# Kernel optimization log

Measured on AMD Instinct MI355X. Metric: run time of the kernel, lower is better.

Reference implementation:

```python
import jax, jax.numpy as jnp
import numpy as np

DIM, HEADS, DEPTH, SEQ, LOCAL_W = 1024, 16, 7, 2048, 64
HEAD_DIM = DIM // HEADS
SCALE = 1.0 / HEAD_DIM ** 0.5


def cantor_mask(S, depth, local_window):
    """Allowed (i,j): |i-j| within local window, OR |i-j| lies in the Cantor set
    under `depth` levels of ternary subdivision (no base-3 digit equals 1)."""
    idx = np.arange(S)
    d = np.abs(idx[:, None] - idx[None, :])
    x = d.copy()
    ok = np.ones_like(d, dtype=bool)
    for _ in range(depth):
        ok &= (x % 3) != 1
        x //= 3
    ok &= x == 0  # offset must be < 3**depth
    return jnp.asarray(ok | (d <= local_window))  # [S, S] bool


def setup_inputs() -> dict:
    key = jax.random.key(0)
    ks = jax.random.split(key, 8)
    B = 2
    s = 0.02
    return {
        "query": jax.random.normal(ks[0], (B, SEQ, DIM), jnp.float32),
        "key_value": jax.random.normal(ks[1], (B, SEQ, DIM), jnp.float32),
        "Wq": jax.random.normal(ks[2], (DIM, DIM), jnp.float32) * s,
        "bq": jnp.zeros((DIM,), jnp.float32),
        "Wkv": jax.random.normal(ks[3], (DIM, 2 * DIM), jnp.float32) * s,
        "bkv": jnp.zeros((2 * DIM,), jnp.float32),
        "Wo": jax.random.normal(ks[4], (DIM, DIM), jnp.float32) * s,
        "bo": jnp.zeros((DIM,), jnp.float32),
    }


def reference(query, key_value, Wq, bq, Wkv, bkv, Wo, bo):
    B, S, D = query.shape
    H, hd = HEADS, HEAD_DIM
    mask = cantor_mask(S, DEPTH, LOCAL_W)  # static [S, S] bool

    q = (query @ Wq + bq).reshape(B, S, H, hd).transpose(0, 2, 1, 3)  # [B,H,S,hd]
    kv = (key_value @ Wkv + bkv).reshape(B, S, 2, H, hd).transpose(2, 0, 3, 1, 4)
    k, v = kv[0], kv[1]  # [B,H,S,hd]

    scores = jnp.einsum("bhqd,bhkd->bhqk", q, k) * SCALE
    scores = jnp.where(mask, scores, jnp.finfo(scores.dtype).min)
    attn = jax.nn.softmax(scores, axis=-1)
    out = jnp.einsum("bhqk,bhkd->bhqd", attn, v)  # [B,H,S,hd]
    out = out.transpose(0, 2, 1, 3).reshape(B, S, D)
    return out @ Wo + bo
```

## Files before the change

kernel.cpp:

```cpp
#include <hip/hip_runtime.h>
#include <stdint.h>

typedef _Float16 half_t;
typedef __attribute__((ext_vector_type(8))) _Float16 half8;
typedef __attribute__((ext_vector_type(4))) _Float16 half4;
typedef __attribute__((ext_vector_type(4))) float floatx4;

#define SEQ 2048
#define NH 16
#define HD 64

#define MFMA16(a, b, c) __builtin_amdgcn_mfma_f32_16x16x16f16(a, b, c, 0, 0, 0)
#define MFMA32K(a, b, c) __builtin_amdgcn_mfma_f32_16x16x32_f16(a, b, c, 0, 0, 0)

#define QSCALE 0.1803368801111306f

__global__ __launch_bounds__(256) void prep(
    const float* __restrict__ query, const float* __restrict__ key_value,
    const float* __restrict__ Wq, const float* __restrict__ Wkv,
    const float* __restrict__ Wo, half_t* __restrict__ xq,
    half_t* __restrict__ xkv, half_t* __restrict__ wqT,
    half_t* __restrict__ wkvT, half_t* __restrict__ woT,
    uint8_t* __restrict__ tok, uint8_t* __restrict__ tok16,
    uint64_t* __restrict__ maskw) {
  int bx = blockIdx.x, tid = threadIdx.x;
  if (bx < 2048) {
    const float* s; half_t* d; int base;
    if (bx < 1024) { s = query; d = xq; base = bx * 4096; }
    else { s = key_value; d = xkv; base = (bx - 1024) * 4096; }
#pragma unroll
    for (int u = 0; u < 4; ++u) {
      int i = base + u * 1024 + tid * 4;
      floatx4 v = *(const floatx4*)(s + i);
      half4 h;
      h[0] = (half_t)v[0]; h[1] = (half_t)v[1];
      h[2] = (half_t)v[2]; h[3] = (half_t)v[3];
      *(half4*)(d + i) = h;
    }
    return;
  }
  if (bx < 4096) {
    __shared__ float tile[32][33];
    int tx = tid & 31, ty = tid >> 5;
    const int K = 1024;
#pragma unroll
    for (int u = 0; u < 2; ++u) {
      int t = (bx - 2048) * 2 + u;
      const float* W; half_t* Wt; int N, nt, kt;
      if (t < 1024) { W = Wq; Wt = wqT; N = 1024; nt = t & 31; kt = t >> 5; }
      else if (t < 3072) { int t2 = t - 1024; W = Wkv; Wt = wkvT; N = 2048; nt = t2 & 63; kt = t2 >> 6; }
      else { int t2 = t - 3072; W = Wo; Wt = woT; N = 1024; nt = t2 & 31; kt = t2 >> 5; }
      int n0 = nt * 32, k0 = kt * 32;
#pragma unroll
      for (int i = 0; i < 4; ++i)
        tile[ty + i * 8][tx] = W[(size_t)(k0 + ty + i * 8) * N + n0 + tx];
      __syncthreads();
#pragma unroll
      for (int i = 0; i < 4; ++i)
        Wt[(size_t)(n0 + ty + i * 8) * K + k0 + tx] = (half_t)tile[tx][ty + i * 8];
      __syncthreads();
    }
    return;
  }
  __shared__ uint8_t slut[2048];
  int ib = bx - 4096;
  for (int d = tid; d < 2048; d += 256) {
    int x = d;
    bool ok = true;
    for (int it = 0; it < 7; ++it) { ok &= ((x % 3) != 1); x /= 3; }
    ok &= (x == 0);
    slut[d] = (ok || d <= 64) ? 1 : 0;
  }
  __syncthreads();
  if (ib == 0) {
    if (tid < 64) {
      int delta = tid - 32;
      int lo = delta * 64 - 63, hi = delta * 64 + 63;
      uint8_t any = 0;
      for (int x = lo; x <= hi; ++x) {
        int a = x < 0 ? -x : x;
        if (a < 2048) any |= slut[a];
      }
      tok[tid] = any;
    }
    {
      int d16 = tid - 128;
      int ctr = d16 * 16;
      uint8_t any = 0;
      for (int x = ctr - 15; x <= ctr + 15; ++x) {
        int a = x < 0 ? -x : x;
        if (a < 2048) any |= slut[a];
      }
      tok16[tid] = any;
    }
  }
  int g = ib * 256 + tid;
  int tt = g - 2048;
  uint64_t w = 0;
  for (int jj = 0; jj < 64; ++jj) {
    int d = tt - jj; d = d < 0 ? -d : d;
    if (d < 2048 && slut[d]) w |= (1ull << jj);
  }
  maskw[g] = w;
}

__device__ __forceinline__ void cp16(half_t* lds, const half_t* g) {
  __builtin_amdgcn_global_load_lds(
      (const __attribute__((address_space(1))) uint32_t*)g,
      (__attribute__((address_space(3))) uint32_t*)lds, 16, 0, 0);
}

__global__ __launch_bounds__(256) void gemm_qkv(
    const half_t* __restrict__ xq, const half_t* __restrict__ xkv,
    const half_t* __restrict__ wqT, const half_t* __restrict__ wkvT,
    const float* __restrict__ bq, const float* __restrict__ bkv,
    half_t* __restrict__ qout, half_t* __restrict__ kout,
    half_t* __restrict__ vTout) {
  extern __shared__ char smemraw[];
  half_t* As = (half_t*)smemraw;
  half_t* Bs = As + 8192;
  const int K = 1024;
  bool isq = blockIdx.y < 8;
  const half_t* A = isq ? xq : xkv;
  const half_t* Bt = isq ? wqT : wkvT;
  const float* bias = isq ? bq : bkv;
  int n0 = (isq ? blockIdx.y : (blockIdx.y - 8)) * 128;
  int m0 = blockIdx.x * 128;

  int tid = threadIdx.x;
  int wave = tid >> 6, lane = tid & 63;
  int c = lane & 15, quad = lane >> 4;
  int wm = (wave >> 1) * 64, wn = (wave & 1) * 64;

  floatx4 acc[4][4] = {};
  int arow = tid >> 2, akc = (tid & 3) * 8;

  cp16(&As[wave * 512], A + (size_t)(m0 + arow) * K + akc);
  cp16(&As[2048 + wave * 512], A + (size_t)(m0 + 64 + arow) * K + akc);
  cp16(&Bs[wave * 512], Bt + (size_t)(n0 + arow) * K + akc);
  cp16(&Bs[2048 + wave * 512], Bt + (size_t)(n0 + 64 + arow) * K + akc);

  for (int kt = 0; kt < 32; ++kt) {
    __syncthreads();
    if (kt + 1 < 32) {
      int k0 = (kt + 1) * 32;
      int b = (kt + 1) & 1;
      cp16(&As[b * 4096 + wave * 512], A + (size_t)(m0 + arow) * K + k0 + akc);
      cp16(&As[b * 4096 + 2048 + wave * 512], A + (size_t)(m0 + 64 + arow) * K + k0 + akc);
      cp16(&Bs[b * 4096 + wave * 512], Bt + (size_t)(n0 + arow) * K + k0 + akc);
      cp16(&Bs[b * 4096 + 2048 + wave * 512], Bt + (size_t)(n0 + 64 + arow) * K + k0 + akc);
    }
    int b = kt & 1;
    half8 af[4], bf[4];
#pragma unroll
    for (int mt = 0; mt < 4; ++mt)
      af[mt] = *(const half8*)&As[b * 4096 + (wm + mt * 16 + c) * 32 + quad * 8];
#pragma unroll
    for (int nt = 0; nt < 4; ++nt)
      bf[nt] = *(const half8*)&Bs[b * 4096 + (wn + nt * 16 + c) * 32 + quad * 8];
#pragma unroll
    for (int mt = 0; mt < 4; ++mt)
#pragma unroll
      for (int nt = 0; nt < 4; ++nt)
        acc[mt][nt] = MFMA32K(af[mt], bf[nt], acc[mt][nt]);
  }

  __syncthreads();
  half_t* ep = (half_t*)smemraw;
  int bb = m0 >> 11, sbase = m0 & 2047;
  bool isv = (!isq) && (n0 >= 1024);

  if (!isv) {
#pragma unroll
    for (int nt = 0; nt < 4; ++nt) {
      int nl = wn + nt * 16 + c;
      float bv = bias[n0 + nl];
#pragma unroll
      for (int mt = 0; mt < 4; ++mt)
#pragma unroll
        for (int r = 0; r < 4; ++r) {
          int ml = wm + mt * 16 + quad * 4 + r;
          float v = acc[mt][nt][r] + bv;
          if (isq) v *= QSCALE;
          ep[ml * 128 + nl] = (half_t)v;
        }
    }
    __syncthreads();
    half_t* outp = isq ? qout : kout;
#pragma unroll
    for (int rd = 0; rd < 8; ++rd) {
      int id = rd * 256 + tid;
      int ml = id >> 4, ch = id & 15;
      int ng = n0 + ch * 8;
      int h = ng >> 6, d0 = ng & 63;
      half8 v = *(const half8*)&ep[ml * 128 + ch * 8];
      *(half8*)(outp + ((size_t)(bb * 16 + h) * SEQ + sbase + ml) * 64 + d0) = v;
    }
  } else {
#pragma unroll
    for (int nt = 0; nt < 4; ++nt) {
      int nl = wn + nt * 16 + c;
      float bv = bias[n0 + nl];
#pragma unroll
      for (int mt = 0; mt < 4; ++mt) {
        int ml = wm + mt * 16 + quad * 4;
        half4 hv;
#pragma unroll
        for (int r = 0; r < 4; ++r) hv[r] = (half_t)(acc[mt][nt][r] + bv);
        *(half4*)&ep[nl * 136 + ml] = hv;
      }
    }
    __syncthreads();
#pragma unroll
    for (int rd = 0; rd < 8; ++rd) {
      int id = rd * 256 + tid;
      int nl = id >> 4, mc = id & 15;
      int ng = n0 + nl;
      int h = (ng >> 6) & 15, d = ng & 63;
      half8 v = *(const half8*)&ep[nl * 136 + mc * 8];
      *(half8*)(vTout + ((size_t)(bb * 16 + h) * 64 + d) * SEQ + sbase + mc * 8) = v;
    }
  }
}

__global__ __launch_bounds__(256) void gemm_out(
    const half_t* __restrict__ A, const half_t* __restrict__ Bt,
    const float* __restrict__ bias, float* __restrict__ outf) {
  __shared__ half_t As[2][128 * 32];
  __shared__ half_t Bs[2][64 * 32];
  const int K = 1024;
  int tid = threadIdx.x;
  int wave = tid >> 6, lane = tid & 63;
  int c = lane & 15, quad = lane >> 4;
  int wm = (wave >> 1) * 64, wn = (wave & 1) * 32;
  int m0 = blockIdx.x * 128, n0 = blockIdx.y * 64;

  floatx4 acc[4][2] = {};
  int arow = tid >> 2, akc = (tid & 3) * 8;

  cp16(&As[0][wave * 512], A + (size_t)(m0 + arow) * K + akc);
  cp16(&As[0][2048 + wave * 512], A + (size_t)(m0 + 64 + arow) * K + akc);
  cp16(&Bs[0][wave * 512], Bt + (size_t)(n0 + arow) * K + akc);

  for (int kt = 0; kt < 32; ++kt) {
    __syncthreads();
    if (kt + 1 < 32) {
      int k0 = (kt + 1) * 32;
      int b = (kt + 1) & 1;
      cp16(&As[b][wave * 512], A + (size_t)(m0 + arow) * K + k0 + akc);
      cp16(&As[b][2048 + wave * 512], A + (size_t)(m0 + 64 + arow) * K + k0 + akc);
      cp16(&Bs[b][wave * 512], Bt + (size_t)(n0 + arow) * K + k0 + akc);
    }
    int b = kt & 1;
    half8 af[4], bf[2];
#pragma unroll
    for (int mt = 0; mt < 4; ++mt)
      af[mt] = *(const half8*)&As[b][(wm + mt * 16 + c) * 32 + quad * 8];
#pragma unroll
    for (int nt = 0; nt < 2; ++nt)
      bf[nt] = *(const half8*)&Bs[b][(wn + nt * 16 + c) * 32 + quad * 8];
#pragma unroll
    for (int mt = 0; mt < 4; ++mt)
#pragma unroll
      for (int nt = 0; nt < 2; ++nt)
        acc[mt][nt] = MFMA32K(af[mt], bf[nt], acc[mt][nt]);
  }

#pragma unroll
  for (int nt = 0; nt < 2; ++nt) {
    int n = n0 + wn + nt * 16 + c;
    float bv = bias[n];
#pragma unroll
    for (int mt = 0; mt < 4; ++mt)
#pragma unroll
      for (int r = 0; r < 4; ++r) {
        int m = m0 + wm + mt * 16 + quad * 4 + r;
        outf[(size_t)m * 1024 + n] = acc[mt][nt][r] + bv;
      }
  }
}

__global__ __launch_bounds__(512) void attn_kernel(
    const half_t* __restrict__ qb, const half_t* __restrict__ kb,
    const half_t* __restrict__ vTg, half_t* __restrict__ ctx,
    const uint64_t* __restrict__ maskw, const uint8_t* __restrict__ tok,
    const uint8_t* __restrict__ tok16g) {
  __shared__ half_t kT[64 * 64];
  __shared__ half_t vT[64 * 64];
  __shared__ half_t ot[128 * 72];
  __shared__ int list[34];
  __shared__ uint8_t tok16s[256];

  int tid = threadIdx.x, wave = tid >> 6, lane = tid & 63;
  int c = lane & 15, q = lane >> 4;
  int id = blockIdx.x;
  int bh = (id & 7) * 4 + ((id >> 3) & 3);
  int it128 = id >> 5;
  int i0 = it128 << 7;
  const half_t* qbase = qb + (size_t)bh * SEQ * HD;
  const half_t* kg = kb + (size_t)bh * SEQ * HD;
  const half_t* vg = vTg + (size_t)bh * HD * SEQ;

  if (tid < 256) tok16s[tid] = tok16g[tid];
  if (wave == 0) {
    int jt = lane;
    int base = i0 >> 6;
    bool act = (jt < 32) &&
               (tok[(jt - base) + 32] | tok[(jt - base - 1) + 32]);
    unsigned long long bal = __ballot(act);
    if (act) {
      int pre = __popcll(bal & ((1ull << jt) - 1));
      list[1 + pre] = jt << 6;
    }
    if (lane == 0) list[0] = __popcll(bal);
  }

  int i_row = i0 + wave * 16 + c;
  int it16 = (i0 >> 4) + wave;
  half8 qf0 = *(const half8*)(qbase + (size_t)i_row * 64 + q * 8);
  half8 qf1 = *(const half8*)(qbase + (size_t)i_row * 64 + 32 + q * 8);

  floatx4 oacc[4] = {};
  floatx4 lacc = {};
  half4 ones;
  ones[0] = (half_t)1.f; ones[1] = (half_t)1.f;
  ones[2] = (half_t)1.f; ones[3] = (half_t)1.f;

  int srow = tid >> 3;
  int sch = tid & 7;
  int ssw = srow & 7;

  __syncthreads();
  int nact = list[0];
  int j0 = list[1];

  half8 kr = *(const half8*)(kg + (size_t)(j0 + srow) * 64 + sch * 8);
  half8 vr = *(const half8*)(vg + (size_t)srow * SEQ + j0 + sch * 8);

  for (int ti = 0; ti < nact; ++ti) {
    uint64_t w = maskw[(i_row - j0) + 2048];
    int bidx = (j0 >> 4) - it16 + 128;
    __syncthreads();
    *(half8*)&kT[srow * 64 + ((sch ^ ssw) * 8)] = kr;
    *(half8*)&vT[srow * 64 + ((sch ^ ssw) * 8)] = vr;
    int j0n = j0;
    if (ti + 1 < nact) {
      j0n = list[2 + ti];
      kr = *(const half8*)(kg + (size_t)(j0n + srow) * 64 + sch * 8);
      vr = *(const half8*)(vg + (size_t)srow * SEQ + j0n + sch * 8);
    }
    __syncthreads();

    uint32_t wlo = (uint32_t)(w >> (4 * q));
    uint32_t whi = (uint32_t)(w >> (32 + 4 * q));
#pragma unroll
    for (int jt = 0; jt < 4; ++jt) {
      if (!tok16s[bidx + jt]) continue;
      int row = jt * 16 + c;
      int sw = c & 7;
      half8 a0 = *(const half8*)&kT[row * 64 + ((q ^ sw) * 8)];
      half8 a1 = *(const half8*)&kT[row * 64 + (((4 + q) ^ sw) * 8)];
      floatx4 t = {};
      t = MFMA32K(a0, qf0, t);
      t = MFMA32K(a1, qf1, t);
      uint32_t ww = (jt < 2) ? wlo : whi;
#pragma unroll
      for (int r = 0; r < 4; ++r) {
        float p = __builtin_exp2f(t[r]);
        int bitpos = 16 * (jt & 1) + r;
        uint32_t msk = (uint32_t)(((int)(ww << (31 - bitpos))) >> 31);
        t[r] = __uint_as_float(__float_as_uint(p) & msk);
      }
      auto lo = __builtin_amdgcn_cvt_pkrtz(t[0], t[1]);
      auto hi = __builtin_amdgcn_cvt_pkrtz(t[2], t[3]);
      half4 pb;
      pb[0] = lo[0]; pb[1] = lo[1]; pb[2] = hi[0]; pb[3] = hi[1];
      lacc = MFMA16(ones, pb, lacc);
#pragma unroll
      for (int mt = 0; mt < 4; ++mt) {
        int drow = mt * 16 + c;
        int ch = 2 * jt + (q >> 1);
        half4 a = *(const half4*)&vT[drow * 64 + ((ch ^ sw) * 8) + (q & 1) * 4];
        oacc[mt] = MFMA16(a, pb, oacc[mt]);
      }
    }
    j0 = j0n;
  }

  float inv_l = 1.0f / lacc[0];
#pragma unroll
  for (int mt = 0; mt < 4; ++mt)
#pragma unroll
    for (int r = 0; r < 4; ++r)
      ot[(wave * 16 + c) * 72 + mt * 16 + 4 * q + r] = (half_t)(oacc[mt][r] * inv_l);
  __syncthreads();
  {
    int row = tid >> 2, chq = tid & 3;
    int b = bh >> 4, h = bh & 15;
    size_t base = (((size_t)(b * SEQ + i0 + row) * NH) + h) * 64 + chq * 16;
    half8 v0 = *(const half8*)&ot[row * 72 + chq * 16];
    half8 v1 = *(const half8*)&ot[row * 72 + chq * 16 + 8];
    *(half8*)(ctx + base) = v0;
    *(half8*)(ctx + base + 8) = v1;
  }
}

extern "C" void kernel_launch(void* const* d_in, const int* in_sizes, int n_in,
                              void* d_out, int out_size, void* d_ws, size_t ws_size,
                              hipStream_t stream) {
  const float* query = (const float*)d_in[0];
  const float* key_value = (const float*)d_in[1];
  const float* Wq = (const float*)d_in[2];
  const float* bq = (const float*)d_in[3];
  const float* Wkv = (const float*)d_in[4];
  const float* bkv = (const float*)d_in[5];
  const float* Wo = (const float*)d_in[6];
  const float* bo = (const float*)d_in[7];

  char* ws = (char*)d_ws;
  uint8_t* tok = (uint8_t*)ws;
  uint8_t* tok16 = (uint8_t*)(ws + 1024);
  uint64_t* maskw = (uint64_t*)(ws + 4096);
  const size_t MB = 1ull << 20;
  half_t* xq = (half_t*)(ws + 1 * MB);
  half_t* xkv = (half_t*)(ws + 9 * MB);
  half_t* wqT = (half_t*)(ws + 17 * MB);
  half_t* wkvT = (half_t*)(ws + 19 * MB);
  half_t* woT = (half_t*)(ws + 23 * MB);
  half_t* qbuf = (half_t*)(ws + 25 * MB);
  half_t* kbuf = (half_t*)(ws + 33 * MB);
  half_t* vTg = (half_t*)(ws + 41 * MB);
  half_t* ctx = xq;

  hipLaunchKernelGGL(prep, dim3(4112), dim3(256), 0, stream,
                     query, key_value, Wq, Wkv, Wo, xq, xkv, wqT, wkvT, woT,
                     tok, tok16, maskw);
  hipLaunchKernelGGL(gemm_qkv, dim3(32, 24), dim3(256), 34816, stream,
                     xq, xkv, wqT, wkvT, bq, bkv, qbuf, kbuf, vTg);
  hipLaunchKernelGGL(attn_kernel, dim3(512), dim3(512), 0, stream,
                     qbuf, kbuf, vTg, ctx, maskw, tok, tok16);
  hipLaunchKernelGGL(gemm_out, dim3(32, 16), dim3(256), 0, stream,
                     ctx, woT, bo, (float*)d_out);
}
```

Baseline: 218.1 us.

## Swizzle GEMM LDS tiles, halve attention block rows, and use mask LUT

The LDS tiles in both GEMMs now have their 16-byte k-chunks XOR-swizzled by row, which is meant to remove bank conflicts on the MFMA fragment loads. The attention kernel now uses 64-row query blocks of 256 threads on a 1024-block grid, with a new block-to-(bh, chunk) mapping meant to improve XCD locality and load balance. Each query block now only visits key tiles active for its own 64-row chunk rather than the union over two chunks. Per-element mask shifts are replaced by a small shared-memory lookup that ANDs packed fp16 pairs. In exchange, each thread now loads twice as many K and V fragments per step, and there are more blocks overall.

Result: slower. 224.3 us (+2.9%).

```diff
diff --git a/kernel.cpp b/kernel.cpp
--- a/kernel.cpp
+++ b/kernel.cpp
@@ -133,7 +133,9 @@
   int wm = (wave >> 1) * 64, wn = (wave & 1) * 64;
 
   floatx4 acc[4][4] = {};
-  int arow = tid >> 2, akc = (tid & 3) * 8;
+  int arow = tid >> 2;
+  int akc = ((tid & 3) ^ (arow & 3)) * 8;
+  int csw = c & 3;
 
   cp16(&As[wave * 512], A + (size_t)(m0 + arow) * K + akc);
   cp16(&As[2048 + wave * 512], A + (size_t)(m0 + 64 + arow) * K + akc);
@@ -154,10 +156,10 @@
     half8 af[4], bf[4];
 #pragma unroll
     for (int mt = 0; mt < 4; ++mt)
-      af[mt] = *(const half8*)&As[b * 4096 + (wm + mt * 16 + c) * 32 + quad * 8];
+      af[mt] = *(const half8*)&As[b * 4096 + (wm + mt * 16 + c) * 32 + ((quad ^ csw) * 8)];
 #pragma unroll
     for (int nt = 0; nt < 4; ++nt)
-      bf[nt] = *(const half8*)&Bs[b * 4096 + (wn + nt * 16 + c) * 32 + quad * 8];
+      bf[nt] = *(const half8*)&Bs[b * 4096 + (wn + nt * 16 + c) * 32 + ((quad ^ csw) * 8)];
 #pragma unroll
     for (int mt = 0; mt < 4; ++mt)
 #pragma unroll
@@ -236,7 +238,9 @@
   int m0 = blockIdx.x * 128, n0 = blockIdx.y * 64;
 
   floatx4 acc[4][2] = {};
-  int arow = tid >> 2, akc = (tid & 3) * 8;
+  int arow = tid >> 2;
+  int akc = ((tid & 3) ^ (arow & 3)) * 8;
+  int csw = c & 3;
 
   cp16(&As[0][wave * 512], A + (size_t)(m0 + arow) * K + akc);
   cp16(&As[0][2048 + wave * 512], A + (size_t)(m0 + 64 + arow) * K + akc);
@@ -255,10 +259,10 @@
     half8 af[4], bf[2];
 #pragma unroll
     for (int mt = 0; mt < 4; ++mt)
-      af[mt] = *(const half8*)&As[b][(wm + mt * 16 + c) * 32 + quad * 8];
+      af[mt] = *(const half8*)&As[b][(wm + mt * 16 + c) * 32 + ((quad ^ csw) * 8)];
 #pragma unroll
     for (int nt = 0; nt < 2; ++nt)
-      bf[nt] = *(const half8*)&Bs[b][(wn + nt * 16 + c) * 32 + quad * 8];
+      bf[nt] = *(const half8*)&Bs[b][(wn + nt * 16 + c) * 32 + ((quad ^ csw) * 8)];
 #pragma unroll
     for (int mt = 0; mt < 4; ++mt)
 #pragma unroll
@@ -280,33 +284,37 @@
   }
 }
 
-__global__ __launch_bounds__(512) void attn_kernel(
+__global__ __launch_bounds__(256) void attn_kernel(
     const half_t* __restrict__ qb, const half_t* __restrict__ kb,
     const half_t* __restrict__ vTg, half_t* __restrict__ ctx,
     const uint64_t* __restrict__ maskw, const uint8_t* __restrict__ tok,
     const uint8_t* __restrict__ tok16g) {
   __shared__ half_t kT[64 * 64];
   __shared__ half_t vT[64 * 64];
-  __shared__ half_t ot[128 * 72];
+  __shared__ half_t ot[64 * 72];
   __shared__ int list[34];
   __shared__ uint8_t tok16s[256];
+  __shared__ uint32_t mlut[16][2];
 
   int tid = threadIdx.x, wave = tid >> 6, lane = tid & 63;
   int c = lane & 15, q = lane >> 4;
   int id = blockIdx.x;
-  int bh = (id & 7) * 4 + ((id >> 3) & 3);
-  int it128 = id >> 5;
-  int i0 = it128 << 7;
+  int xcd = id & 7, s = (id >> 3) & 31, bhq = id >> 8;
+  int bh = xcd * 4 + bhq;
+  int chunk = ((s & 7) << 2) | (s >> 3);
+  int i0 = chunk << 6;
   const half_t* qbase = qb + (size_t)bh * SEQ * HD;
   const half_t* kg = kb + (size_t)bh * SEQ * HD;
   const half_t* vg = vTg + (size_t)bh * HD * SEQ;
 
-  if (tid < 256) tok16s[tid] = tok16g[tid];
+  tok16s[tid] = tok16g[tid];
+  if (tid < 16) {
+    mlut[tid][0] = (tid & 1 ? 0xFFFFu : 0u) | (tid & 2 ? 0xFFFF0000u : 0u);
+    mlut[tid][1] = (tid & 4 ? 0xFFFFu : 0u) | (tid & 8 ? 0xFFFF0000u : 0u);
+  }
   if (wave == 0) {
     int jt = lane;
-    int base = i0 >> 6;
-    bool act = (jt < 32) &&
-               (tok[(jt - base) + 32] | tok[(jt - base - 1) + 32]);
+    bool act = (jt < 32) && tok[(jt - chunk) + 32];
     unsigned long long bal = __ballot(act);
     if (act) {
       int pre = __popcll(bal & ((1ull << jt) - 1));
@@ -326,28 +334,36 @@
   ones[0] = (half_t)1.f; ones[1] = (half_t)1.f;
   ones[2] = (half_t)1.f; ones[3] = (half_t)1.f;
 
-  int srow = tid >> 3;
-  int sch = tid & 7;
+  int srow = tid >> 2;
+  int sc0 = (tid & 3) * 2;
   int ssw = srow & 7;
+  int slotA = (sc0 ^ ssw) * 8;
+  int slotB = ((sc0 + 1) ^ ssw) * 8;
 
   __syncthreads();
   int nact = list[0];
   int j0 = list[1];
 
-  half8 kr = *(const half8*)(kg + (size_t)(j0 + srow) * 64 + sch * 8);
-  half8 vr = *(const half8*)(vg + (size_t)srow * SEQ + j0 + sch * 8);
+  half8 krA = *(const half8*)(kg + (size_t)(j0 + srow) * 64 + sc0 * 8);
+  half8 krB = *(const half8*)(kg + (size_t)(j0 + srow) * 64 + sc0 * 8 + 8);
+  half8 vrA = *(const half8*)(vg + (size_t)srow * SEQ + j0 + sc0 * 8);
+  half8 vrB = *(const half8*)(vg + (size_t)srow * SEQ + j0 + sc0 * 8 + 8);
 
   for (int ti = 0; ti < nact; ++ti) {
     uint64_t w = maskw[(i_row - j0) + 2048];
     int bidx = (j0 >> 4) - it16 + 128;
     __syncthreads();
-    *(half8*)&kT[srow * 64 + ((sch ^ ssw) * 8)] = kr;
-    *(half8*)&vT[srow * 64 + ((sch ^ ssw) * 8)] = vr;
+    *(half8*)&kT[srow * 64 + slotA] = krA;
+    *(half8*)&kT[srow * 64 + slotB] = krB;
+    *(half8*)&vT[srow * 64 + slotA] = vrA;
+    *(half8*)&vT[srow * 64 + slotB] = vrB;
     int j0n = j0;
     if (ti + 1 < nact) {
       j0n = list[2 + ti];
-      kr = *(const half8*)(kg + (size_t)(j0n + srow) * 64 + sch * 8);
-      vr = *(const half8*)(vg + (size_t)srow * SEQ + j0n + sch * 8);
+      krA = *(const half8*)(kg + (size_t)(j0n + srow) * 64 + sc0 * 8);
+      krB = *(const half8*)(kg + (size_t)(j0n + srow) * 64 + sc0 * 8 + 8);
+      vrA = *(const half8*)(vg + (size_t)srow * SEQ + j0n + sc0 * 8);
+      vrB = *(const half8*)(vg + (size_t)srow * SEQ + j0n + sc0 * 8 + 8);
     }
     __syncthreads();
 
@@ -364,17 +380,19 @@
       t = MFMA32K(a0, qf0, t);
       t = MFMA32K(a1, qf1, t);
       uint32_t ww = (jt < 2) ? wlo : whi;
-#pragma unroll
-      for (int r = 0; r < 4; ++r) {
-        float p = __builtin_exp2f(t[r]);
-        int bitpos = 16 * (jt & 1) + r;
-        uint32_t msk = (uint32_t)(((int)(ww << (31 - bitpos))) >> 31);
-        t[r] = __uint_as_float(__float_as_uint(p) & msk);
-      }
-      auto lo = __builtin_amdgcn_cvt_pkrtz(t[0], t[1]);
-      auto hi = __builtin_amdgcn_cvt_pkrtz(t[2], t[3]);
-      half4 pb;
-      pb[0] = lo[0]; pb[1] = lo[1]; pb[2] = hi[0]; pb[3] = hi[1];
+      uint32_t nib = (ww >> (16 * (jt & 1))) & 15u;
+      uint32_t m01 = mlut[nib][0];
+      uint32_t m23 = mlut[nib][1];
+      float p0 = __builtin_exp2f(t[0]);
+      float p1 = __builtin_exp2f(t[1]);
+      float p2 = __builtin_exp2f(t[2]);
+      float p3 = __builtin_exp2f(t[3]);
+      auto lo = __builtin_amdgcn_cvt_pkrtz(p0, p1);
+      auto hi = __builtin_amdgcn_cvt_pkrtz(p2, p3);
+      union { uint32_t u[2]; half4 h4; } pu;
+      pu.u[0] = __builtin_bit_cast(uint32_t, lo) & m01;
+      pu.u[1] = __builtin_bit_cast(uint32_t, hi) & m23;
+      half4 pb = pu.h4;
       lacc = MFMA16(ones, pb, lacc);
 #pragma unroll
       for (int mt = 0; mt < 4; ++mt) {
@@ -437,7 +455,7 @@
                      tok, tok16, maskw);
   hipLaunchKernelGGL(gemm_qkv, dim3(32, 24), dim3(256), 34816, stream,
                      xq, xkv, wqT, wkvT, bq, bkv, qbuf, kbuf, vTg);
-  hipLaunchKernelGGL(attn_kernel, dim3(512), dim3(512), 0, stream,
+  hipLaunchKernelGGL(attn_kernel, dim3(1024), dim3(256), 0, stream,
                      qbuf, kbuf, vTg, ctx, maskw, tok, tok16);
   hipLaunchKernelGGL(gemm_out, dim3(32, 16), dim3(256), 0, stream,
                      ctx, woT, bo, (float*)d_out);
```
